# Optimization experiments

Measured on AMD Instinct MI355X. Metric: run time of the kernel, lower is better.

Reference implementation:

```python
import jax, jax.numpy as jnp
import numpy as np

N, D, DR, DA = 50000, 128, 64, 64
R, A = 2000, 5000
L, H = 2, 2
E, E2, EA = 400000, 800000, 400000


def setup_inputs() -> dict:
    key = jax.random.key(0)
    ks = jax.random.split(key, 8)
    rng = np.random.default_rng(0)

    ee = np.stack([rng.integers(0, N, E), rng.integers(0, N, E)], 1)
    ee = ee[np.lexsort((ee[:, 1], ee[:, 0]))]            # sorted unique-ish ent-ent edges
    seg_id = np.repeat(np.arange(E), 2)                  # 2 relation rows per edge
    er_rel = rng.integers(0, R, E2)
    er_index = np.stack([np.repeat(ee[:, 0], 2), er_rel], 1)   # (node, rel) pairs
    ea_index = np.stack([rng.integers(0, N, EA), rng.integers(0, A, EA)], 1)
    ea_index = ea_index[np.lexsort((ea_index[:, 1], ea_index[:, 0]))]

    s192 = 1.0 / np.sqrt(192.0)
    s320 = 1.0 / np.sqrt(320.0)
    return {
        "ent_emb": jax.random.normal(ks[0], (N, D), jnp.float32) * 0.1,
        "rel_emb": jax.random.normal(ks[1], (R, DR), jnp.float32) * 0.1,
        "attr_emb": jax.random.normal(ks[2], (A, DA), jnp.float32) * 0.1,
        "w_r": jax.random.normal(ks[3], (192, 1), jnp.float32) * s192,
        "b_r": jnp.zeros((1,), jnp.float32),
        "w_a": jax.random.normal(ks[4], (192, 1), jnp.float32) * s192,
        "b_a": jnp.zeros((1,), jnp.float32),
        "ent_attn_w": jax.random.normal(ks[5], (L, H, 192, 1), jnp.float32) * s192,
        "ent_attn_b": jnp.zeros((L, H, 1), jnp.float32),
        "con_attn_w": jax.random.normal(ks[6], (L, H, 320, 1), jnp.float32) * s320,
        "con_attn_b": jnp.zeros((L, H, 1), jnp.float32),
        "ee_index": jnp.asarray(ee, jnp.int32),
        "seg_id": jnp.asarray(seg_id, jnp.int32),
        "er_rel": jnp.asarray(er_rel, jnp.int32),
        "er_index": jnp.asarray(er_index, jnp.int32),
        "ea_index": jnp.asarray(ea_index, jnp.int32),
    }


def _leaky(v):
    return jnp.where(v > 0, v, 0.3 * v)  # LeakyReLU(alpha=0.3)


def _seg_softmax(vals, seg, n):
    m = jax.ops.segment_max(vals, seg, num_segments=n)
    e = jnp.exp(vals - m[seg])
    s = jax.ops.segment_sum(e, seg, num_segments=n)
    return e / s[seg]


def _forward(ent_emb, rel_emb, attr_emb, w_r, b_r, w_a, b_a,
             eaw, eab, caw, cab, ee_index, seg_id, er_rel, er_index, ea_index):
    n, d = ent_emb.shape
    nl, nh = eaw.shape[0], eaw.shape[1]
    dh = d // nh
    ne = ee_index.shape[0]

    def concept(idx, emb, w, b):
        feat = jnp.concatenate([ent_emb[idx[:, 0]], emb[idx[:, 1]]], axis=1)
        a = _leaky(feat @ w + b).reshape(-1)
        p = _seg_softmax(a, idx[:, 0], n)                      # tf.sparse.softmax per row
        return jax.nn.relu(jax.ops.segment_sum(p[:, None] * emb[idx[:, 1]], idx[:, 0], num_segments=n))

    concept_rel = concept(er_index, rel_emb, w_r, b_r)         # (N, DR)
    concept_attr = concept(ea_index, attr_emb, w_a, b_a)       # (N, DA)

    row, col = ee_index[:, 0], ee_index[:, 1]
    # softmax over all-ones sparse adj == neighbor mean
    deg = jax.ops.segment_sum(jnp.ones((ne,), ent_emb.dtype), row, num_segments=n)
    x = jax.ops.segment_sum(ent_emb[col], row, num_segments=n) / jnp.maximum(deg, 1.0)[:, None]

    # segment_mean of relation embeddings over duplicate (h,t) edges
    cnt = jax.ops.segment_sum(jnp.ones((er_rel.shape[0],), ent_emb.dtype), seg_id, num_segments=ne)
    rels_mean = jax.ops.segment_sum(rel_emb[er_rel], seg_id, num_segments=ne) / jnp.maximum(cnt, 1.0)[:, None]

    # concept features per edge (same for every layer/head -> hoisted)
    con_feat = jnp.concatenate([concept_rel[row], concept_attr[row], rels_mean,
                                concept_rel[col], concept_attr[col]], axis=1)  # (E, 320)

    layer_outs = []
    for l in range(nl):
        x = jax.nn.relu(x)
        heads = x.reshape(n, nh, dh)
        outs = []
        for h in range(nh):
            xe = heads[:, h, :]
            nf = xe[col]
            ef = jnp.concatenate([xe[row], rels_mean, nf], axis=1)      # (E, 192)
            ea = _leaky(ef @ eaw[l, h] + eab[l, h]).reshape(-1)
            ca = _leaky(con_feat @ caw[l, h] + cab[l, h]).reshape(-1)
            p = jax.nn.softmax(ea * ca)         # tf.nn.softmax over all edge values
            p = _seg_softmax(p, row, n)          # then tf.sparse.softmax per row
            outs.append(jax.ops.segment_sum(p[:, None] * nf, row, num_segments=n))
        x = jnp.tanh(jnp.concatenate(outs, axis=1))
        layer_outs.append(x)

    grat_out = jnp.concatenate(layer_outs, axis=1)                     # (N, L*D)
    ent_out = jnp.concatenate([grat_out, concept_rel, concept_attr], axis=1)
    conc = jnp.concatenate([concept_rel, concept_attr], axis=1)
    return ent_out, conc


def reference(ent_emb, rel_emb, attr_emb, w_r, b_r, w_a, b_a,
              ent_attn_w, ent_attn_b, con_attn_w, con_attn_b,
              ee_index, seg_id, er_rel, er_index, ea_index):
    return _forward(ent_emb, rel_emb, attr_emb, w_r, b_r, w_a, b_a,
                    ent_attn_w, ent_attn_b, con_attn_w, con_attn_b,
                    ee_index, seg_id, er_rel, er_index, ea_index)
```

## Files before the change

kernel.cpp:

```cpp
#include <hip/hip_runtime.h>
#include <math.h>

#define NENT 50000
#define RREL 2000
#define AATT 5000
#define EE   400000
#define E2   800000
#define EAE  400000
#define PRE_PTR_B   196
#define PRE_SMALL_B 20

__device__ __forceinline__ float leaky(float v){ return v > 0.f ? v : 0.3f * v; }

__device__ __forceinline__ float wave_sum(float v){
#pragma unroll
  for (int m = 32; m; m >>= 1) v += __shfl_xor(v, m);
  return v;
}
__device__ __forceinline__ float sum16(float v){
#pragma unroll
  for (int m = 1; m < 16; m <<= 1) v += __shfl_xor(v, m);
  return v;
}
__device__ __forceinline__ float sum8(float v){
#pragma unroll
  for (int m = 1; m < 8; m <<= 1) v += __shfl_xor(v, m);
  return v;
}

__device__ int lowb(const int* a, int n, int key){
  int lo = 0, hi = n;
  while (lo < hi){ int mid = (lo + hi) >> 1; if (a[2 * mid] < key) lo = mid + 1; else hi = mid; }
  return lo;
}

__global__ void k_pre(const int* ee, const int* er, const int* ea,
                      int* pee, int* per, int* pea,
                      const float* rel_emb, const float* attr_emb,
                      const float* w_r, const float* w_a,
                      const float* eaw, const float* caw,
                      float* h_rel, float* h_attr, float4* HH0, float4* HH1,
                      const float* ent_emb, float* her, float* hea){
  int b = blockIdx.x;
  if (b < PRE_PTR_B){
    int i = b * 256 + threadIdx.x;
    if (i <= NENT){
      pee[i] = lowb(ee, EE, i);
      per[i] = lowb(er, E2, i);
      pea[i] = lowb(ea, EAE, i);
    }
  } else if (b < PRE_PTR_B + PRE_SMALL_B){
    int t = (b - PRE_PTR_B) * 256 + threadIdx.x;
    if (t < RREL){
      const float* e = rel_emb + (size_t)t * 64;
      float s = 0.f;
      for (int k = 0; k < 64; ++k) s += e[k] * w_r[128 + k];
      h_rel[t] = s;
      float hr[4], hc[4];
      for (int lh = 0; lh < 4; ++lh){
        float a = 0.f, c = 0.f;
        for (int k = 0; k < 64; ++k){
          a += e[k] * eaw[lh * 192 + 64 + k];
          c += e[k] * caw[lh * 320 + 128 + k];
        }
        hr[lh] = a; hc[lh] = c;
      }
      HH0[t] = make_float4(hr[0], hr[1], hc[0], hc[1]);
      HH1[t] = make_float4(hr[2], hr[3], hc[2], hc[3]);
    }
    if (t < AATT){
      const float* e = attr_emb + (size_t)t * 64;
      float s = 0.f;
      for (int k = 0; k < 64; ++k) s += e[k] * w_a[128 + k];
      h_attr[t] = s;
    }
  } else {
    int w = (((b - PRE_PTR_B - PRE_SMALL_B) * 256 + (int)threadIdx.x) >> 6);
    int lane = threadIdx.x & 63;
    if (w >= NENT) return;
    float2 v = ((const float2*)(ent_emb + (size_t)w * 128))[lane];
    float2 a = ((const float2*)w_r)[lane];
    float2 bb = ((const float2*)w_a)[lane];
    float sr = wave_sum(v.x * a.x + v.y * a.y);
    float sa = wave_sum(v.x * bb.x + v.y * bb.y);
    if (lane == 0){ her[w] = sr; hea[w] = sa; }
  }
}

__global__ void k_cw(const int* er_idx, const int* ea_idx,
                     const float* her, const float* hea,
                     const float* h_rel, const float* h_attr,
                     const float* b_r, const float* b_a,
                     float* wr, float* wa){
  int e = blockIdx.x * blockDim.x + threadIdx.x;
  if (e < E2){
    int2 rc = ((const int2*)er_idx)[e];
    wr[e] = __expf(leaky(her[rc.x] + h_rel[rc.y] + b_r[0]));
  }
  if (e < EAE){
    int2 rc = ((const int2*)ea_idx)[e];
    wa[e] = __expf(leaky(hea[rc.x] + h_attr[rc.y] + b_a[0]));
  }
}

__device__ float4 concept_g(const float* wq, const int* idx, int beg, int end,
                            const float* emb, int p){
  float t = 0.f;
  for (int e = beg + p; e < end; e += 16) t += wq[e];
  t = sum16(t);
  float invz = (t > 0.f) ? (1.f / t) : 0.f;
  float4 acc = {0.f, 0.f, 0.f, 0.f};
  for (int c0 = beg; c0 < end; c0 += 8){
    int cnt = end - c0; if (cnt > 8) cnt = 8;
#pragma unroll
    for (int j = 0; j < 8; ++j){
      int e = c0 + ((j < cnt) ? j : 0);
      float wgt = wq[e] * invz;
      if (j >= cnt) wgt = 0.f;
      int obj = ((const int2*)idx)[e].y;
      float4 f = ((const float4*)(emb + (size_t)obj * 64))[p];
      acc.x = fmaf(wgt, f.x, acc.x); acc.y = fmaf(wgt, f.y, acc.y);
      acc.z = fmaf(wgt, f.z, acc.z); acc.w = fmaf(wgt, f.w, acc.w);
    }
  }
  acc.x = fmaxf(acc.x, 0.f); acc.y = fmaxf(acc.y, 0.f);
  acc.z = fmaxf(acc.z, 0.f); acc.w = fmaxf(acc.w, 0.f);
  return acc;
}

__global__ void k_phase1(const float* ent_emb, const float* rel_emb, const float* attr_emb,
                         const float* eaw, const float* caw,
                         const int* er_idx, const int* ea_idx, const int* ee,
                         const int* per, const int* pea, const int* pee,
                         const float* wr, const float* wa,
                         float4* UA0, float4* VB0, float4* UA1, float4* VB1,
                         float* out){
  int tid = blockIdx.x * blockDim.x + threadIdx.x;
  int lane = threadIdx.x & 63;
  int p = lane & 15;
  int w = (tid >> 6) * 4 + (lane >> 4);
  if (w >= NENT) return;
  float4 accR = concept_g(wr, er_idx, per[w], per[w + 1], rel_emb, p);
  float4 accA = concept_g(wa, ea_idx, pea[w], pea[w + 1], attr_emb, p);
  ((float4*)(out + (size_t)w * 384 + 256))[p] = accR;
  ((float4*)(out + (size_t)w * 384 + 320))[p] = accA;
  ((float4*)(out + (size_t)NENT * 384 + (size_t)w * 128))[p] = accR;
  ((float4*)(out + (size_t)NENT * 384 + (size_t)w * 128 + 64))[p] = accA;
  int beg = pee[w], end = pee[w + 1];
  float4 mx = {0.f,0.f,0.f,0.f}, my = {0.f,0.f,0.f,0.f};
  for (int c0 = beg; c0 < end; c0 += 4){
    int cnt = end - c0; if (cnt > 4) cnt = 4;
#pragma unroll
    for (int j = 0; j < 4; ++j){
      int e = c0 + ((j < cnt) ? j : 0);
      float msk = (j < cnt) ? 1.f : 0.f;
      int ce = ((const int2*)ee)[e].y;
      const float4* r = (const float4*)(ent_emb + (size_t)ce * 128);
      float4 q0 = r[p], q1 = r[p + 16];
      mx.x = fmaf(msk, q0.x, mx.x); mx.y = fmaf(msk, q0.y, mx.y);
      mx.z = fmaf(msk, q0.z, mx.z); mx.w = fmaf(msk, q0.w, mx.w);
      my.x = fmaf(msk, q1.x, my.x); my.y = fmaf(msk, q1.y, my.y);
      my.z = fmaf(msk, q1.z, my.z); my.w = fmaf(msk, q1.w, my.w);
    }
  }
  float invd = 1.f / fmaxf((float)(end - beg), 1.f);
  mx.x *= invd; mx.y *= invd; mx.z *= invd; mx.w *= invd;
  my.x *= invd; my.y *= invd; my.z *= invd; my.w *= invd;
  ((float4*)(out + (size_t)w * 384 + 128))[p] = mx;
  ((float4*)(out + (size_t)w * 384 + 192))[p] = my;
#pragma unroll
  for (int lh = 0; lh < 4; ++lh){
    const float* cw = caw + lh * 320;
    float4 c0 = *(const float4*)(cw + 4 * p);
    float4 c1 = *(const float4*)(cw + 64 + 4 * p);
    float4 c2 = *(const float4*)(cw + 192 + 4 * p);
    float4 c3 = *(const float4*)(cw + 256 + 4 * p);
    float av = accR.x*c0.x + accR.y*c0.y + accR.z*c0.z + accR.w*c0.w
             + accA.x*c1.x + accA.y*c1.y + accA.z*c1.z + accA.w*c1.w;
    float bv = accR.x*c2.x + accR.y*c2.y + accR.z*c2.z + accR.w*c2.w
             + accA.x*c3.x + accA.y*c3.y + accA.z*c3.z + accA.w*c3.w;
    av = sum16(av); bv = sum16(bv);
    if (p == 0){
      float4* U = (lh < 2) ? UA0 : UA1;
      float4* V = (lh < 2) ? VB0 : VB1;
      ((float*)(U + w))[2 + (lh & 1)] = av;
      ((float*)(V + w))[2 + (lh & 1)] = bv;
    }
  }
  {
    float e0 = fmaxf(mx.x,0.f), e1 = fmaxf(mx.y,0.f), e2 = fmaxf(mx.z,0.f), e3 = fmaxf(mx.w,0.f);
    float e4 = fmaxf(my.x,0.f), e5 = fmaxf(my.y,0.f), e6 = fmaxf(my.z,0.f), e7 = fmaxf(my.w,0.f);
    float4 u0 = *(const float4*)(eaw + 4 * p);
    float4 v0 = *(const float4*)(eaw + 128 + 4 * p);
    float4 u1 = *(const float4*)(eaw + 192 + 4 * p);
    float4 v1 = *(const float4*)(eaw + 192 + 128 + 4 * p);
    float pu0 = sum16(e0*u0.x + e1*u0.y + e2*u0.z + e3*u0.w);
    float pv0 = sum16(e0*v0.x + e1*v0.y + e2*v0.z + e3*v0.w);
    float pu1 = sum16(e4*u1.x + e5*u1.y + e6*u1.z + e7*u1.w);
    float pv1 = sum16(e4*v1.x + e5*v1.y + e6*v1.z + e7*v1.w);
    if (p == 0){
      ((float*)(UA0 + w))[0] = pu0; ((float*)(UA0 + w))[1] = pu1;
      ((float*)(VB0 + w))[0] = pv0; ((float*)(VB0 + w))[1] = pv1;
    }
  }
}

__global__ void k_se(const int* ee, const int* err,
                     const float4* UA, const float4* VB, const float4* HH,
                     const float* eab_l, const float* cab_l, float2* s01){
  int e = blockIdx.x * blockDim.x + threadIdx.x;
  if (e >= EE) return;
  int2 rc = ((const int2*)ee)[e];
  int2 rr = ((const int2*)err)[e];
  float4 ua = UA[rc.x], vb = VB[rc.y], h1 = HH[rr.x], h2 = HH[rr.y];
  float ea0 = ua.x + 0.5f * (h1.x + h2.x) + vb.x + eab_l[0];
  float ca0 = ua.z + 0.5f * (h1.z + h2.z) + vb.z + cab_l[0];
  float ex0 = __expf(leaky(ea0) * leaky(ca0));
  float ea1 = ua.y + 0.5f * (h1.y + h2.y) + vb.y + eab_l[1];
  float ca1 = ua.w + 0.5f * (h1.w + h2.w) + vb.w + cab_l[1];
  float ex1 = __expf(leaky(ea1) * leaky(ca1));
  s01[e] = make_float2(ex0, ex1);
}

__global__ void k_agg(const int* ee, const int* ptr, const float2* q01,
                      const float* xsrc, float* outp, int ocol,
                      const float* eaw_next, float4* UAn, float4* VBn){
  int tid = blockIdx.x * blockDim.x + threadIdx.x;
  int lane = threadIdx.x & 63;
  int p = lane & 15;
  int w = (tid >> 6) * 4 + (lane >> 4);
  if (w >= NENT) return;
  int beg = ptr[w], end = ptr[w + 1];
  const float invZ = 1.0f / (float)EE;
  float4 a0 = {0.f,0.f,0.f,0.f}, a1 = {0.f,0.f,0.f,0.f};
  float4 b0 = {0.f,0.f,0.f,0.f}, b1 = {0.f,0.f,0.f,0.f};
  float T = 0.f;
  for (int c0 = beg; c0 < end; c0 += 8){
    int cnt = end - c0; if (cnt > 8) cnt = 8;
#pragma unroll
    for (int j = 0; j < 8; ++j){
      int e = c0 + ((j < cnt) ? j : 0);
      float2 q = q01[e];
      float s = (p < 8) ? q.x : q.y;
      if (j >= cnt) s = 0.f;
      float msk = (j < cnt) ? 1.f : 0.f;
      T += s;
      int cj = ((const int2*)ee)[e].y;
      const float4* r = (const float4*)(xsrc + (size_t)cj * 384);
      float4 f0 = r[2 * p], f1 = r[2 * p + 1];
      f0.x = fmaxf(f0.x, 0.f); f0.y = fmaxf(f0.y, 0.f);
      f0.z = fmaxf(f0.z, 0.f); f0.w = fmaxf(f0.w, 0.f);
      f1.x = fmaxf(f1.x, 0.f); f1.y = fmaxf(f1.y, 0.f);
      f1.z = fmaxf(f1.z, 0.f); f1.w = fmaxf(f1.w, 0.f);
      b0.x = fmaf(msk, f0.x, b0.x); b0.y = fmaf(msk, f0.y, b0.y);
      b0.z = fmaf(msk, f0.z, b0.z); b0.w = fmaf(msk, f0.w, b0.w);
      b1.x = fmaf(msk, f1.x, b1.x); b1.y = fmaf(msk, f1.y, b1.y);
      b1.z = fmaf(msk, f1.z, b1.z); b1.w = fmaf(msk, f1.w, b1.w);
      a0.x = fmaf(s, f0.x, a0.x); a0.y = fmaf(s, f0.y, a0.y);
      a0.z = fmaf(s, f0.z, a0.z); a0.w = fmaf(s, f0.w, a0.w);
      a1.x = fmaf(s, f1.x, a1.x); a1.y = fmaf(s, f1.y, a1.y);
      a1.z = fmaf(s, f1.z, a1.z); a1.w = fmaf(s, f1.w, a1.w);
    }
  }
  float cnt = (float)(end - beg);
  float denom = cnt + invZ * T;
  float inv = (end > beg) ? (1.f / denom) : 0.f;
  float4 o0, o1;
  o0.x = tanhf((b0.x + invZ * a0.x) * inv); o0.y = tanhf((b0.y + invZ * a0.y) * inv);
  o0.z = tanhf((b0.z + invZ * a0.z) * inv); o0.w = tanhf((b0.w + invZ * a0.w) * inv);
  o1.x = tanhf((b1.x + invZ * a1.x) * inv); o1.y = tanhf((b1.y + invZ * a1.y) * inv);
  o1.z = tanhf((b1.z + invZ * a1.z) * inv); o1.w = tanhf((b1.w + invZ * a1.w) * inv);
  ((float4*)(outp + (size_t)w * 384 + ocol))[2 * p]     = o0;
  ((float4*)(outp + (size_t)w * 384 + ocol))[2 * p + 1] = o1;
  if (eaw_next){
    float e0 = fmaxf(o0.x,0.f), e1 = fmaxf(o0.y,0.f), e2 = fmaxf(o0.z,0.f), e3 = fmaxf(o0.w,0.f);
    float e4 = fmaxf(o1.x,0.f), e5 = fmaxf(o1.y,0.f), e6 = fmaxf(o1.z,0.f), e7 = fmaxf(o1.w,0.f);
    int hh = p >> 3;
    int dbase = (8 * p) & 63;
    const float* wvp = eaw_next + hh * 192;
    float4 u0 = *(const float4*)(wvp + dbase);
    float4 u1 = *(const float4*)(wvp + dbase + 4);
    float4 q0 = *(const float4*)(wvp + 128 + dbase);
    float4 q1 = *(const float4*)(wvp + 128 + dbase + 4);
    float pu = e0*u0.x + e1*u0.y + e2*u0.z + e3*u0.w
             + e4*u1.x + e5*u1.y + e6*u1.z + e7*u1.w;
    float pv = e0*q0.x + e1*q0.y + e2*q0.z + e3*q0.w
             + e4*q1.x + e5*q1.y + e6*q1.z + e7*q1.w;
    pu = sum8(pu); pv = sum8(pv);
    if (p == 0 || p == 8){
      ((float*)(UAn + w))[hh] = pu;
      ((float*)(VBn + w))[hh] = pv;
    }
  }
}

extern "C" void kernel_launch(void* const* d_in, const int* in_sizes, int n_in,
                              void* d_out, int out_size, void* d_ws, size_t ws_size,
                              hipStream_t stream){
  const float* ent_emb  = (const float*)d_in[0];
  const float* rel_emb  = (const float*)d_in[1];
  const float* attr_emb = (const float*)d_in[2];
  const float* w_r      = (const float*)d_in[3];
  const float* b_r      = (const float*)d_in[4];
  const float* w_a      = (const float*)d_in[5];
  const float* b_a      = (const float*)d_in[6];
  const float* eaw      = (const float*)d_in[7];
  const float* eab      = (const float*)d_in[8];
  const float* caw      = (const float*)d_in[9];
  const float* cab      = (const float*)d_in[10];
  const int*   ee       = (const int*)d_in[11];
  const int*   er_rel2  = (const int*)d_in[13];
  const int*   er_idx   = (const int*)d_in[14];
  const int*   ea_idx   = (const int*)d_in[15];
  float* out = (float*)d_out;

  int* pee = (int*)d_ws;
  int* per = pee + (NENT + 1);
  int* pea = per + (NENT + 1);
  float*  fbase = (float*)d_ws + 150004;
  float4* UA0 = (float4*)fbase;
  float4* VB0 = UA0 + NENT;
  float4* UA1 = VB0 + NENT;
  float4* VB1 = UA1 + NENT;
  float4* HH0 = VB1 + NENT;
  float4* HH1 = HH0 + RREL;
  float* her     = (float*)(HH1 + RREL);
  float* hea     = her + NENT;
  float* h_rel   = hea + NENT;
  float* h_attr  = h_rel + RREL;
  float* wr      = h_attr + AATT;
  float* wa      = wr + E2;
  float2* s01    = (float2*)wr;

  const int nb = (EE + 255) / 256;
  const int gq = (NENT + 15) / 16;
  const int npre = PRE_PTR_B + PRE_SMALL_B + (NENT * 64 + 255) / 256;

  k_pre<<<npre, 256, 0, stream>>>(ee, er_idx, ea_idx, pee, per, pea,
                                  rel_emb, attr_emb, w_r, w_a, eaw, caw,
                                  h_rel, h_attr, HH0, HH1, ent_emb, her, hea);
  k_cw<<<(E2 + 255) / 256, 256, 0, stream>>>(er_idx, ea_idx, her, hea,
                                             h_rel, h_attr, b_r, b_a, wr, wa);
  k_phase1<<<gq, 256, 0, stream>>>(ent_emb, rel_emb, attr_emb, eaw, caw,
                                   er_idx, ea_idx, ee, per, pea, pee, wr, wa,
                                   UA0, VB0, UA1, VB1, out);
  k_se<<<nb, 256, 0, stream>>>(ee, er_rel2, UA0, VB0, HH0, eab, cab, s01);
  k_agg<<<gq, 256, 0, stream>>>(ee, pee, s01, out + 128, out, 0,
                                eaw + 2 * 192, UA1, VB1);
  k_se<<<nb, 256, 0, stream>>>(ee, er_rel2, UA1, VB1, HH1, eab + 2, cab + 2, s01);
  k_agg<<<gq, 256, 0, stream>>>(ee, pee, s01, out, out, 128,
                                (const float*)nullptr, (float4*)nullptr, (float4*)nullptr);
}
```

Measured before the change: 178.7 us.

## Fuse concept-weight computation into phase1 and stage weights in LDS

Removes the separate k_cw kernel that wrote per-edge exp(leaky) weights for relation and attribute edges to global memory. k_phase1 now computes those weights on the fly from the per-node and per-table scores, caching the first 64 weights and object ids per node in shared memory for the aggregation pass. This saves one launch and a global write/read round trip of about 1.2M floats. Edges beyond 64 per node get their exp recomputed, and the kernel now uses 8KB of shared memory per block.

```diff
diff --git a/kernel.cpp b/kernel.cpp
--- a/kernel.cpp
+++ b/kernel.cpp
@@ -87,37 +87,32 @@
   }
 }
 
-__global__ void k_cw(const int* er_idx, const int* ea_idx,
-                     const float* her, const float* hea,
-                     const float* h_rel, const float* h_attr,
-                     const float* b_r, const float* b_a,
-                     float* wr, float* wa){
-  int e = blockIdx.x * blockDim.x + threadIdx.x;
-  if (e < E2){
-    int2 rc = ((const int2*)er_idx)[e];
-    wr[e] = __expf(leaky(her[rc.x] + h_rel[rc.y] + b_r[0]));
-  }
-  if (e < EAE){
-    int2 rc = ((const int2*)ea_idx)[e];
-    wa[e] = __expf(leaky(hea[rc.x] + h_attr[rc.y] + b_a[0]));
-  }
-}
-
-__device__ float4 concept_g(const float* wq, const int* idx, int beg, int end,
-                            const float* emb, int p){
+__device__ float4 concept_g(float he, const float* h_tab, const int* idx,
+                            int beg, int end, const float* emb, int p,
+                            float* swq, int* sobj){
+  int len = end - beg;
   float t = 0.f;
-  for (int e = beg + p; e < end; e += 16) t += wq[e];
+  for (int k = p; k < len; k += 16){
+    int obj = ((const int2*)idx)[beg + k].y;
+    float wq = __expf(leaky(he + h_tab[obj]));
+    if (k < 64){ swq[k] = wq; sobj[k] = obj; }
+    t += wq;
+  }
   t = sum16(t);
   float invz = (t > 0.f) ? (1.f / t) : 0.f;
   float4 acc = {0.f, 0.f, 0.f, 0.f};
-  for (int c0 = beg; c0 < end; c0 += 8){
-    int cnt = end - c0; if (cnt > 8) cnt = 8;
+  for (int c0 = 0; c0 < len; c0 += 8){
+    int cnt = len - c0; if (cnt > 8) cnt = 8;
 #pragma unroll
     for (int j = 0; j < 8; ++j){
-      int e = c0 + ((j < cnt) ? j : 0);
-      float wgt = wq[e] * invz;
-      if (j >= cnt) wgt = 0.f;
-      int obj = ((const int2*)idx)[e].y;
+      int k = c0 + ((j < cnt) ? j : 0);
+      int obj; float wq;
+      if (k < 64){ obj = sobj[k]; wq = swq[k]; }
+      else {
+        obj = ((const int2*)idx)[beg + k].y;
+        wq = __expf(leaky(he + h_tab[obj]));
+      }
+      float wgt = (j < cnt) ? wq * invz : 0.f;
       float4 f = ((const float4*)(emb + (size_t)obj * 64))[p];
       acc.x = fmaf(wgt, f.x, acc.x); acc.y = fmaf(wgt, f.y, acc.y);
       acc.z = fmaf(wgt, f.z, acc.z); acc.w = fmaf(wgt, f.w, acc.w);
@@ -132,16 +127,23 @@
                          const float* eaw, const float* caw,
                          const int* er_idx, const int* ea_idx, const int* ee,
                          const int* per, const int* pea, const int* pee,
-                         const float* wr, const float* wa,
+                         const float* her, const float* hea,
+                         const float* h_rel, const float* h_attr,
+                         const float* b_r, const float* b_a,
                          float4* UA0, float4* VB0, float4* UA1, float4* VB1,
                          float* out){
+  __shared__ float swq[16][64];
+  __shared__ int   sobj[16][64];
   int tid = blockIdx.x * blockDim.x + threadIdx.x;
   int lane = threadIdx.x & 63;
   int p = lane & 15;
+  int g = threadIdx.x >> 4;
   int w = (tid >> 6) * 4 + (lane >> 4);
   if (w >= NENT) return;
-  float4 accR = concept_g(wr, er_idx, per[w], per[w + 1], rel_emb, p);
-  float4 accA = concept_g(wa, ea_idx, pea[w], pea[w + 1], attr_emb, p);
+  float heR = her[w] + b_r[0];
+  float heA = hea[w] + b_a[0];
+  float4 accR = concept_g(heR, h_rel, er_idx, per[w], per[w + 1], rel_emb, p, swq[g], sobj[g]);
+  float4 accA = concept_g(heA, h_attr, ea_idx, pea[w], pea[w + 1], attr_emb, p, swq[g], sobj[g]);
   ((float4*)(out + (size_t)w * 384 + 256))[p] = accR;
   ((float4*)(out + (size_t)w * 384 + 320))[p] = accA;
   ((float4*)(out + (size_t)NENT * 384 + (size_t)w * 128))[p] = accR;
@@ -328,9 +330,7 @@
   float* hea     = her + NENT;
   float* h_rel   = hea + NENT;
   float* h_attr  = h_rel + RREL;
-  float* wr      = h_attr + AATT;
-  float* wa      = wr + E2;
-  float2* s01    = (float2*)wr;
+  float2* s01    = (float2*)(h_attr + AATT);
 
   const int nb = (EE + 255) / 256;
   const int gq = (NENT + 15) / 16;
@@ -339,10 +339,9 @@
   k_pre<<<npre, 256, 0, stream>>>(ee, er_idx, ea_idx, pee, per, pea,
                                   rel_emb, attr_emb, w_r, w_a, eaw, caw,
                                   h_rel, h_attr, HH0, HH1, ent_emb, her, hea);
-  k_cw<<<(E2 + 255) / 256, 256, 0, stream>>>(er_idx, ea_idx, her, hea,
-                                             h_rel, h_attr, b_r, b_a, wr, wa);
   k_phase1<<<gq, 256, 0, stream>>>(ent_emb, rel_emb, attr_emb, eaw, caw,
-                                   er_idx, ea_idx, ee, per, pea, pee, wr, wa,
+                                   er_idx, ea_idx, ee, per, pea, pee,
+                                   her, hea, h_rel, h_attr, b_r, b_a,
                                    UA0, VB0, UA1, VB1, out);
   k_se<<<nb, 256, 0, stream>>>(ee, er_rel2, UA0, VB0, HH0, eab, cab, s01);
   k_agg<<<gq, 256, 0, stream>>>(ee, pee, s01, out + 128, out, 0,
```

Result: no change. 176.9 us (-1.0%).
